# Kernel tuning notes

Hardware: AMD Instinct MI355X
Metric: run time of the kernel (lower is better)

The kernel has to match this reference:

```python
import jax, jax.numpy as jnp
from jax import lax
import numpy as np

PAD = 99          # padding_token from __init__
EPS = 1e-7        # keras backend epsilon used by ctc_batch_cost
NEG = jnp.float32(-1e30)


def setup_inputs() -> dict:
    key = jax.random.key(0)
    k1, k2, k3 = jax.random.split(key, 3)
    B, T, C, L = 512, 512, 81, 64
    # y_pred: softmax probabilities, as ctc_batch_cost expects
    y_pred = jax.nn.softmax(jax.random.normal(k1, (B, T, C), jnp.float32), axis=-1)
    labels = jax.random.randint(k2, (B, L), 0, C - 1)            # chars in [0, 79], blank=80
    lengths = jax.random.randint(k3, (B,), 16, L + 1)            # label lengths in [16, 64]
    pos = jnp.arange(L)
    y_true = jnp.where(pos[None, :] < lengths[:, None], labels, PAD).astype(jnp.int32)
    return {"y_true": y_true, "y_pred": y_pred}


def _ctc_loss(log_probs, labels, label_length, blank):
    # log_probs [B,T,C]; labels [B,L] (already de-padded to valid ids); label_length [B]
    B, T, C = log_probs.shape
    L = labels.shape[1]
    S = 2 * L + 1
    # extended label sequence: blank, l1, blank, l2, ..., blank
    ext = jnp.full((B, S), blank, labels.dtype).at[:, 1::2].set(labels)        # [B,S]
    # emission log-probs gathered per extended-label position: [B,T,S]
    lp_ext = jnp.take_along_axis(log_probs[:, :, None, :], ext[:, None, :, None], axis=3)[..., 0]
    s_idx = jnp.arange(S)
    valid = s_idx[None, :] < (2 * label_length[:, None] + 1)                   # [B,S]
    ext_m2 = jnp.pad(ext, ((0, 0), (2, 0)), constant_values=blank)[:, :S]
    allow_skip = (ext != blank) & (ext != ext_m2)                              # [B,S]

    alpha0 = jnp.full((B, S), NEG)
    alpha0 = alpha0.at[:, 0].set(lp_ext[:, 0, 0])
    alpha0 = alpha0.at[:, 1].set(lp_ext[:, 0, 1])
    alpha0 = jnp.where(valid, alpha0, NEG)

    def step(alpha, lp_t):
        a1 = alpha
        a2 = jnp.pad(alpha, ((0, 0), (1, 0)), constant_values=NEG)[:, :S]
        a3 = jnp.where(allow_skip, jnp.pad(alpha, ((0, 0), (2, 0)), constant_values=NEG)[:, :S], NEG)
        m = jnp.maximum(jnp.maximum(a1, a2), a3)
        new = m + jnp.log(jnp.exp(a1 - m) + jnp.exp(a2 - m) + jnp.exp(a3 - m)) + lp_t
        new = jnp.where(valid, new, NEG)
        return new, None

    lp_seq = jnp.swapaxes(lp_ext, 0, 1)        # [T,B,S]
    alpha_T, _ = lax.scan(step, alpha0, lp_seq[1:])
    # total log-likelihood: sum of paths ending at last blank or last label
    e1 = 2 * label_length                       # index of final blank
    e2 = jnp.maximum(2 * label_length - 1, 0)   # index of final label
    a1 = jnp.take_along_axis(alpha_T, e1[:, None], axis=1)[:, 0]
    a2 = jnp.take_along_axis(alpha_T, e2[:, None], axis=1)[:, 0]
    m = jnp.maximum(a1, a2)
    ll = m + jnp.log(jnp.exp(a1 - m) + jnp.exp(a2 - m))
    return -ll


def reference(y_true, y_pred):
    # Faithful to CTCLayer.call: compute input_length=T for all, label_length from
    # padding mask, then ctc_batch_cost(y_true, y_pred, ...). Returns the per-example
    # loss [B,1] (the quantity stashed via add_loss; layer passes y_pred through).
    B, T, C = y_pred.shape
    blank = C - 1                               # TF v1 ctc_loss default blank index
    mask = y_true != PAD
    label_length = jnp.sum(mask.astype(jnp.int32), axis=1)     # [B]
    labels = jnp.where(mask, y_true, 0)
    log_probs = jnp.log(y_pred + EPS)
    loss = _ctc_loss(log_probs, labels, label_length, blank)
    return loss[:, None]                        # [B,1] like ctc_batch_cost
```

## Files before the change

kernel.cpp:

```cpp
#include <hip/hip_runtime.h>


#define TSTEPS 512
#define NCLS   81
#define ROWB   324
#define LMAX   64
#define PADTOK 99
#define EPSF   1e-7f
#define UU     8
#define CHB    (UU * ROWB)

#if __has_builtin(__builtin_amdgcn_logf)
#define FLOG2 __builtin_amdgcn_logf
#else
#define FLOG2 log2f
#endif

__device__ __forceinline__ double dpp_shr1_f64(double x) {
  unsigned long long u = __builtin_bit_cast(unsigned long long, x);
  int lo = __builtin_amdgcn_update_dpp(0, (int)u,         0x138, 0xF, 0xF, true);
  int hi = __builtin_amdgcn_update_dpp(0, (int)(u >> 32), 0x138, 0xF, 0xF, true);
  unsigned long long r = ((unsigned long long)(unsigned)hi << 32) | (unsigned)lo;
  return __builtin_bit_cast(double, r);
}

template <int CTRL>
__device__ __forceinline__ int dppmaxi(int x) {
  int y = __builtin_amdgcn_update_dpp(0, x, CTRL, 0xF, 0xF, true);
  return x > y ? x : y;
}

__device__ __forceinline__ double andm(double x, long long m) {
  return __builtin_bit_cast(double, __builtin_bit_cast(long long, x) & m);
}

#define GL(dst, p, OFF) \
  asm volatile("global_load_dword %0, %1, off offset:" #OFF : "=v"(dst) : "v"(p))

#define LOADC(BB, LL) do { \
    GL(BB[0], pbp, 0);    GL(LL[0], plp, 0); \
    GL(BB[1], pbp, 324);  GL(LL[1], plp, 324); \
    GL(BB[2], pbp, 648);  GL(LL[2], plp, 648); \
    GL(BB[3], pbp, 972);  GL(LL[3], plp, 972); \
    GL(BB[4], pbp, 1296); GL(LL[4], plp, 1296); \
    GL(BB[5], pbp, 1620); GL(LL[5], plp, 1620); \
    GL(BB[6], pbp, 1944); GL(LL[6], plp, 1944); \
    GL(BB[7], pbp, 2268); GL(LL[7], plp, 2268); \
    pbp += CHB; plp += CHB; \
  } while (0)

#define WAITV(N) asm volatile("s_waitcnt vmcnt(" #N ")" ::: "memory")

#define PIN(BB, LL) \
  asm volatile("" : "+v"(BB[0]), "+v"(BB[1]), "+v"(BB[2]), "+v"(BB[3]), \
                    "+v"(BB[4]), "+v"(BB[5]), "+v"(BB[6]), "+v"(BB[7]), \
                    "+v"(LL[0]), "+v"(LL[1]), "+v"(LL[2]), "+v"(LL[3]), \
                    "+v"(LL[4]), "+v"(LL[5]), "+v"(LL[6]), "+v"(LL[7]))

#define STEP(pbv, plv) do { \
    const double qb  = (double)((pbv) + EPSF); \
    const double ql  = (double)((plv) + EPSF); \
    const double a1u = dpp_shr1_f64(a1); \
    const double a3  = andm(a1u, allowm); \
    const double n0  = (a0 + a1u) * qb; \
    const double n1  = andm(((a1 + a0) + a3) * ql, validm); \
    if (full) a2 = (a2 + a1) * qb; \
    a0 = n0; a1 = n1; \
  } while (0)

#define COMP(BB, LL) do { \
    _Pragma("unroll") \
    for (int u = 0; u < UU; ++u) STEP(BB[u], LL[u]); \
  } while (0)

#define RESCALE do { \
    double mx = fmax(fmax(a0, a1), a2); \
    int mh = (int)(__builtin_bit_cast(unsigned long long, mx) >> 32); \
    mh = dppmaxi<0x111>(mh); \
    mh = dppmaxi<0x112>(mh); \
    mh = dppmaxi<0x114>(mh); \
    mh = dppmaxi<0x118>(mh); \
    mh = dppmaxi<0x142>(mh); \
    mh = dppmaxi<0x143>(mh); \
    const int hb = __builtin_amdgcn_readlane(mh, 63); \
    const int ef = (hb >> 20) & 0x7FF; \
    const double sc = __builtin_bit_cast(double, \
                        (unsigned long long)(2046 - ef) << 52); \
    a0 *= sc; a1 *= sc; a2 *= sc; \
    Esum += ef - 1023; \
  } while (0)

__global__ __launch_bounds__(64, 1) void ctc_kernel(
    const int* __restrict__ y_true, const float* __restrict__ y_pred,
    float* __restrict__ out)
{
  const int b    = blockIdx.x;
  const int lane = threadIdx.x;
  const char* yp = (const char*)(y_pred + (size_t)b * (TSTEPS * NCLS));

  const int  yt  = y_true[b * LMAX + lane];
  const bool mk  = (yt != PADTOK);
  const int  len = __popcll(__ballot(mk));
  const int  lab = mk ? yt : 0;
  const int  labu = __shfl_up(lab, 1);
  const long long allowm = ((lane >= 1) && (lab != labu)) ? -1LL : 0LL;
  const long long validm = (lane < len) ? -1LL : 0LL;
  const bool lane0 = (lane == 0);
  const bool full  = (len == LMAX);

  const char* pbp = yp + 320;
  const char* plp = yp + lab * 4;

  double a0, a1, a2;
  int Esum = 0;
  float bA[UU], lA[UU], bB[UU], lB[UU], bC[UU], lC[UU], bD[UU], lD[UU];

  LOADC(bA, lA);
  LOADC(bB, lB);
  LOADC(bC, lC);

  WAITV(32); PIN(bA, lA); LOADC(bD, lD);
  {
    a0 = lane0 ? (double)(bA[0] + EPSF) : 0.0;
    a1 = lane0 ? (double)(lA[0] + EPSF) : 0.0;
    a2 = 0.0;
#pragma unroll
    for (int u = 1; u < UU; ++u) STEP(bA[u], lA[u]);
  }
  WAITV(32); PIN(bB, lB); LOADC(bA, lA); COMP(bB, lB);
  WAITV(32); PIN(bC, lC); LOADC(bB, lB); COMP(bC, lC);
  WAITV(32); PIN(bD, lD); LOADC(bC, lC); COMP(bD, lD);
  RESCALE;

#pragma unroll 1
  for (int i = 1; i < 15; ++i) {
    WAITV(32); PIN(bA, lA); LOADC(bD, lD); COMP(bA, lA);
    WAITV(32); PIN(bB, lB); LOADC(bA, lA); COMP(bB, lB);
    WAITV(32); PIN(bC, lC); LOADC(bB, lB); COMP(bC, lC);
    WAITV(32); PIN(bD, lD); LOADC(bC, lC); COMP(bD, lD);
    RESCALE;
  }

  WAITV(32); PIN(bA, lA); LOADC(bD, lD); COMP(bA, lA);
  WAITV(32); PIN(bB, lB); COMP(bB, lB);
  WAITV(16); PIN(bC, lC); COMP(bC, lC);
  WAITV(0);  PIN(bD, lD); COMP(bD, lD);

  const double x1 = full ? __shfl(a2, 63) : __shfl(a0, len);
  const double x2 = __shfl(a1, len - 1);
  const double s  = x1 + x2;
  const unsigned long long sb = __builtin_bit_cast(unsigned long long, s);
  const int    e2   = (int)((sb >> 52) & 0x7FF) - 1023;
  const double mant = __builtin_bit_cast(double,
      (sb & 0x000FFFFFFFFFFFFFULL) | 0x3FF0000000000000ULL);
  const float  ll2  = FLOG2((float)mant) + (float)(e2 + Esum);
  if (lane0) out[b] = -ll2 * 0.69314718055994530942f;
}

extern "C" void kernel_launch(void* const* d_in, const int* in_sizes, int n_in,
                              void* d_out, int out_size, void* d_ws, size_t ws_size,
                              hipStream_t stream) {
  const int*   y_true = (const int*)d_in[0];
  const float* y_pred = (const float*)d_in[1];
  float*       out    = (float*)d_out;
  hipLaunchKernelGGL(ctc_kernel, dim3(512), dim3(64), 0, stream,
                     y_true, y_pred, out);
}
```

Measured before the change: 28.92 us.

## Split CTC recursion into forward and backward halves on two wavefronts

Runs the alpha (forward) recursion over the first half of the time steps on one wavefront and a beta (backward) recursion over the second half on a second wavefront, then combines them through shared memory with a dot product and wave reduction. The aim is to roughly halve the serial dependency chain per batch element, which bounds latency in this one-wave-per-block kernel. It adds a block barrier, LDS traffic and a more complex backward step with extra DPP shifts. It also drops the conditional on the full-length path, and any bug in the time split or in the exponent bookkeeping would change the result.

```diff
diff --git a/kernel.cpp b/kernel.cpp
--- a/kernel.cpp
+++ b/kernel.cpp
@@ -23,13 +23,18 @@
   unsigned long long r = ((unsigned long long)(unsigned)hi << 32) | (unsigned)lo;
   return __builtin_bit_cast(double, r);
 }
-
+__device__ __forceinline__ double dpp_shl1_f64(double x) {
+  unsigned long long u = __builtin_bit_cast(unsigned long long, x);
+  int lo = __builtin_amdgcn_update_dpp(0, (int)u,         0x130, 0xF, 0xF, true);
+  int hi = __builtin_amdgcn_update_dpp(0, (int)(u >> 32), 0x130, 0xF, 0xF, true);
+  unsigned long long r = ((unsigned long long)(unsigned)hi << 32) | (unsigned)lo;
+  return __builtin_bit_cast(double, r);
+}
 template <int CTRL>
 __device__ __forceinline__ int dppmaxi(int x) {
   int y = __builtin_amdgcn_update_dpp(0, x, CTRL, 0xF, 0xF, true);
   return x > y ? x : y;
 }
-
 __device__ __forceinline__ double andm(double x, long long m) {
   return __builtin_bit_cast(double, __builtin_bit_cast(long long, x) & m);
 }
@@ -37,7 +42,7 @@
 #define GL(dst, p, OFF) \
   asm volatile("global_load_dword %0, %1, off offset:" #OFF : "=v"(dst) : "v"(p))
 
-#define LOADC(BB, LL) do { \
+#define LOADBODY(BB, LL) \
     GL(BB[0], pbp, 0);    GL(LL[0], plp, 0); \
     GL(BB[1], pbp, 324);  GL(LL[1], plp, 324); \
     GL(BB[2], pbp, 648);  GL(LL[2], plp, 648); \
@@ -45,9 +50,10 @@
     GL(BB[4], pbp, 1296); GL(LL[4], plp, 1296); \
     GL(BB[5], pbp, 1620); GL(LL[5], plp, 1620); \
     GL(BB[6], pbp, 1944); GL(LL[6], plp, 1944); \
-    GL(BB[7], pbp, 2268); GL(LL[7], plp, 2268); \
-    pbp += CHB; plp += CHB; \
-  } while (0)
+    GL(BB[7], pbp, 2268); GL(LL[7], plp, 2268);
+
+#define LOADCF(BB, LL) do { LOADBODY(BB, LL) pbp += CHB; plp += CHB; } while (0)
+#define LOADCB(BB, LL) do { LOADBODY(BB, LL) pbp -= CHB; plp -= CHB; } while (0)
 
 #define WAITV(N) asm volatile("s_waitcnt vmcnt(" #N ")" ::: "memory")
 
@@ -57,24 +63,38 @@
                     "+v"(LL[0]), "+v"(LL[1]), "+v"(LL[2]), "+v"(LL[3]), \
                     "+v"(LL[4]), "+v"(LL[5]), "+v"(LL[6]), "+v"(LL[7]))
 
-#define STEP(pbv, plv) do { \
+#define STEPF(pbv, plv) do { \
     const double qb  = (double)((pbv) + EPSF); \
     const double ql  = (double)((plv) + EPSF); \
     const double a1u = dpp_shr1_f64(a1); \
     const double a3  = andm(a1u, allowm); \
     const double n0  = (a0 + a1u) * qb; \
     const double n1  = andm(((a1 + a0) + a3) * ql, validm); \
-    if (full) a2 = (a2 + a1) * qb; \
+    a2 = (a2 + a1) * qb; \
     a0 = n0; a1 = n1; \
   } while (0)
 
-#define COMP(BB, LL) do { \
-    _Pragma("unroll") \
-    for (int u = 0; u < UU; ++u) STEP(BB[u], LL[u]); \
-  } while (0)
-
-#define RESCALE do { \
-    double mx = fmax(fmax(a0, a1), a2); \
+#define STEPB(pbv, plv) do { \
+    const double qb = (double)((pbv) + EPSF); \
+    const double ql = (double)((plv) + EPSF); \
+    const double d0 = g0 * qb; \
+    const double d1 = g1 * ql; \
+    const double d2 = g2 * qb; \
+    const double s0 = dpp_shl1_f64(d0); \
+    const double s1 = dpp_shl1_f64(d1); \
+    const double t1 = (d1 + (s0 + andm(d2, l63m))) + andm(s1, am_next); \
+    g1 = andm(t1, validm); \
+    g0 = d0 + d1; \
+    g2 = d2; \
+  } while (0)
+
+#define COMPF(BB, LL) do { \
+    _Pragma("unroll") for (int u = 0; u < UU; ++u) STEPF(BB[u], LL[u]); } while (0)
+#define COMPB(BB, LL) do { \
+    _Pragma("unroll") for (int u = UU - 1; u >= 0; --u) STEPB(BB[u], LL[u]); } while (0)
+
+#define RESCALE3(x, y, z, E) do { \
+    double mx = fmax(fmax(x, y), z); \
     int mh = (int)(__builtin_bit_cast(unsigned long long, mx) >> 32); \
     mh = dppmaxi<0x111>(mh); \
     mh = dppmaxi<0x112>(mh); \
@@ -86,75 +106,105 @@
     const int ef = (hb >> 20) & 0x7FF; \
     const double sc = __builtin_bit_cast(double, \
                         (unsigned long long)(2046 - ef) << 52); \
-    a0 *= sc; a1 *= sc; a2 *= sc; \
-    Esum += ef - 1023; \
-  } while (0)
-
-__global__ __launch_bounds__(64, 1) void ctc_kernel(
+    x *= sc; y *= sc; z *= sc; \
+    E += ef - 1023; \
+  } while (0)
+
+#define DRIVER(LOADM, COMPM, INITM, RESCM) do { \
+    LOADM(bA, lA); LOADM(bB, lB); LOADM(bC, lC); \
+    WAITV(32); PIN(bA, lA); LOADM(bD, lD); INITM; \
+    WAITV(32); PIN(bB, lB); LOADM(bA, lA); COMPM(bB, lB); \
+    WAITV(32); PIN(bC, lC); LOADM(bB, lB); COMPM(bC, lC); \
+    WAITV(32); PIN(bD, lD); LOADM(bC, lC); COMPM(bD, lD); RESCM; \
+    _Pragma("unroll 1") \
+    for (int i = 1; i < 7; ++i) { \
+      WAITV(32); PIN(bA, lA); LOADM(bD, lD); COMPM(bA, lA); \
+      WAITV(32); PIN(bB, lB); LOADM(bA, lA); COMPM(bB, lB); \
+      WAITV(32); PIN(bC, lC); LOADM(bB, lB); COMPM(bC, lC); \
+      WAITV(32); PIN(bD, lD); LOADM(bC, lC); COMPM(bD, lD); RESCM; \
+    } \
+    WAITV(32); PIN(bA, lA); LOADM(bD, lD); COMPM(bA, lA); \
+    WAITV(32); PIN(bB, lB); COMPM(bB, lB); \
+    WAITV(16); PIN(bC, lC); COMPM(bC, lC); \
+    WAITV(0);  PIN(bD, lD); COMPM(bD, lD); RESCM; \
+  } while (0)
+
+#define INITF do { \
+    a0 = lane0 ? (double)(bA[0] + EPSF) : 0.0; \
+    a1 = lane0 ? (double)(lA[0] + EPSF) : 0.0; \
+    a2 = 0.0; \
+    _Pragma("unroll") for (int u = 1; u < UU; ++u) STEPF(bA[u], lA[u]); \
+  } while (0)
+
+#define INITB do { \
+    g0 = (lane == len)     ? 1.0 : 0.0;    \
+    g1 = (lane == len - 1) ? 1.0 : 0.0;    \
+    g2 = (full && lane == 63) ? 1.0 : 0.0;  \
+    _Pragma("unroll") for (int u = UU - 1; u >= 0; --u) STEPB(bA[u], lA[u]); \
+  } while (0)
+
+__global__ __launch_bounds__(128, 1) void ctc_kernel(
     const int* __restrict__ y_true, const float* __restrict__ y_pred,
     float* __restrict__ out)
 {
   const int b    = blockIdx.x;
-  const int lane = threadIdx.x;
+  const int tid  = threadIdx.x;
+  const int lane = tid & 63;
+  const int wv   = tid >> 6;
   const char* yp = (const char*)(y_pred + (size_t)b * (TSTEPS * NCLS));
 
   const int  yt  = y_true[b * LMAX + lane];
   const bool mk  = (yt != PADTOK);
   const int  len = __popcll(__ballot(mk));
   const int  lab = mk ? yt : 0;
-  const int  labu = __shfl_up(lab, 1);
-  const long long allowm = ((lane >= 1) && (lab != labu)) ? -1LL : 0LL;
-  const long long validm = (lane < len) ? -1LL : 0LL;
+  const int  labu   = __shfl_up(lab, 1);
+  const int  allowi = ((lane >= 1) && (lab != labu)) ? 1 : 0;
+  const int  allown = __shfl_down(allowi, 1);
+  const long long allowm  = allowi ? -1LL : 0LL;
+  const long long am_next = allown ? -1LL : 0LL;
+  const long long validm  = (lane < len) ? -1LL : 0LL;
+  const long long l63m    = (lane == 63) ? -1LL : 0LL;
   const bool lane0 = (lane == 0);
   const bool full  = (len == LMAX);
 
-  const char* pbp = yp + 320;
-  const char* plp = yp + lab * 4;
+  __shared__ double sh[129];
+  __shared__ int    shE;
 
   double a0, a1, a2;
-  int Esum = 0;
+  double g0, g1, g2;
+  int Ef = 0, Eb = 0;
   float bA[UU], lA[UU], bB[UU], lB[UU], bC[UU], lC[UU], bD[UU], lD[UU];
 
-  LOADC(bA, lA);
-  LOADC(bB, lB);
-  LOADC(bC, lC);
-
-  WAITV(32); PIN(bA, lA); LOADC(bD, lD);
-  {
-    a0 = lane0 ? (double)(bA[0] + EPSF) : 0.0;
-    a1 = lane0 ? (double)(lA[0] + EPSF) : 0.0;
-    a2 = 0.0;
+  if (wv == 0) {
+    const char* pbp = yp + 320;
+    const char* plp = yp + lab * 4;
+    DRIVER(LOADCF, COMPF, INITF, RESCALE3(a0, a1, a2, Ef));
+    sh[lane]      = a0;
+    sh[64 + lane] = a1;
+    if (lane == 63) sh[128] = a2;
+    if (lane0)      shE     = Ef;
+  } else {
+    const char* pbp = yp + 504 * ROWB + 320;
+    const char* plp = yp + 504 * ROWB + lab * 4;
+    DRIVER(LOADCB, COMPB, INITB, RESCALE3(g0, g1, g2, Eb));
+  }
+
+  __syncthreads();
+
+  if (wv == 1) {
+    double p = g0 * sh[lane] + g1 * sh[64 + lane];
+    p += andm(g2 * sh[128], l63m);
 #pragma unroll
-    for (int u = 1; u < UU; ++u) STEP(bA[u], lA[u]);
+    for (int off = 32; off; off >>= 1) p += __shfl_xor(p, off);
+    if (lane0) {
+      const unsigned long long sb = __builtin_bit_cast(unsigned long long, p);
+      const int    e2   = (int)((sb >> 52) & 0x7FF) - 1023;
+      const double mant = __builtin_bit_cast(double,
+          (sb & 0x000FFFFFFFFFFFFFULL) | 0x3FF0000000000000ULL);
+      const float  ll2  = FLOG2((float)mant) + (float)(e2 + Ef + Eb + shE - Ef);
+      out[b] = -ll2 * 0.69314718055994530942f;
+    }
   }
-  WAITV(32); PIN(bB, lB); LOADC(bA, lA); COMP(bB, lB);
-  WAITV(32); PIN(bC, lC); LOADC(bB, lB); COMP(bC, lC);
-  WAITV(32); PIN(bD, lD); LOADC(bC, lC); COMP(bD, lD);
-  RESCALE;
-
-#pragma unroll 1
-  for (int i = 1; i < 15; ++i) {
-    WAITV(32); PIN(bA, lA); LOADC(bD, lD); COMP(bA, lA);
-    WAITV(32); PIN(bB, lB); LOADC(bA, lA); COMP(bB, lB);
-    WAITV(32); PIN(bC, lC); LOADC(bB, lB); COMP(bC, lC);
-    WAITV(32); PIN(bD, lD); LOADC(bC, lC); COMP(bD, lD);
-    RESCALE;
-  }
-
-  WAITV(32); PIN(bA, lA); LOADC(bD, lD); COMP(bA, lA);
-  WAITV(32); PIN(bB, lB); COMP(bB, lB);
-  WAITV(16); PIN(bC, lC); COMP(bC, lC);
-  WAITV(0);  PIN(bD, lD); COMP(bD, lD);
-
-  const double x1 = full ? __shfl(a2, 63) : __shfl(a0, len);
-  const double x2 = __shfl(a1, len - 1);
-  const double s  = x1 + x2;
-  const unsigned long long sb = __builtin_bit_cast(unsigned long long, s);
-  const int    e2   = (int)((sb >> 52) & 0x7FF) - 1023;
-  const double mant = __builtin_bit_cast(double,
-      (sb & 0x000FFFFFFFFFFFFFULL) | 0x3FF0000000000000ULL);
-  const float  ll2  = FLOG2((float)mant) + (float)(e2 + Esum);
-  if (lane0) out[b] = -ll2 * 0.69314718055994530942f;
 }
 
 extern "C" void kernel_launch(void* const* d_in, const int* in_sizes, int n_in,
@@ -163,6 +213,6 @@
   const int*   y_true = (const int*)d_in[0];
   const float* y_pred = (const float*)d_in[1];
   float*       out    = (float*)d_out;
-  hipLaunchKernelGGL(ctc_kernel, dim3(512), dim3(64), 0, stream,
+  hipLaunchKernelGGL(ctc_kernel, dim3(512), dim3(128), 0, stream,
                      y_true, y_pred, out);
 }
```

Result: faster. 24.59 us (-15.0%).
